# Performance work log

Hardware: AMD Instinct MI355X
Metric: run time of the kernel (lower is better)

## Reference

```python
import jax, jax.numpy as jnp
import numpy as np

BITS = (2, 4, 6, 8, 12, 16)
INIT_S = (0.5, 0.1, 0.05, 0.01, 0.005, 0.001)


def _round_ste(x):
    # straight-through round (LSQ)
    return x + jax.lax.stop_gradient(jnp.round(x) - x)


def _grad_scale(s, g):
    # forward = s, backward grad scaled by g (LSQ grad-scale trick)
    return s * g + jax.lax.stop_gradient(s - s * g)


def _lsq(x, s, num_bits):
    qn = -(2 ** (num_bits - 1))
    qp = 2 ** (num_bits - 1) - 1
    g = 1.0 / float(np.sqrt(x.size * qp))
    ss = _grad_scale(s, g)
    return _round_ste(jnp.clip(x / ss, qn, qp)) * ss


def _gumbel_hard(key, logits, tau):
    u = jax.random.uniform(key, logits.shape, minval=1e-10, maxval=1.0)
    gn = -jnp.log(-jnp.log(u))
    y_soft = jax.nn.softmax((logits + gn) / tau, axis=-1)
    y_hard = jax.nn.one_hot(jnp.argmax(y_soft, axis=-1), logits.shape[-1], dtype=y_soft.dtype)
    return y_hard + y_soft - jax.lax.stop_gradient(y_soft)


def setup_inputs() -> dict:
    key = jax.random.key(0)
    ks = jax.random.split(key, 16)
    B, L, N, K, HD = 64, 256, 8, 64, 64
    inp = {
        "v": jax.random.normal(ks[0], (B, L, K, 2), jnp.float32),
        "H": jax.random.normal(ks[1], (B, L, N, K, 2), jnp.float32),
        "y": jax.random.normal(ks[2], (B, L, N, 2), jnp.float32),
        "local_snr": jax.random.uniform(ks[3], (B, L, K, 1), jnp.float32),
        "w1": jax.random.normal(ks[4], (HD, 9), jnp.float32) * 0.05,
        "b1": jnp.zeros((HD,), jnp.float32),
        "w2": jax.random.normal(ks[5], (HD, HD), jnp.float32) * 0.05,
        "b2": jnp.zeros((HD,), jnp.float32),
        "w3": jax.random.normal(ks[6], (HD, HD), jnp.float32) * 0.05,
        "b3": jnp.zeros((HD,), jnp.float32),
        "wy": jax.random.normal(ks[7], (6, HD), jnp.float32) * 0.05,
        "by": jnp.zeros((6,), jnp.float32),
        "wh": jax.random.normal(ks[8], (6, HD), jnp.float32) * 0.05,
        "bh": jnp.zeros((6,), jnp.float32),
        "wd": jax.random.normal(ks[9], (6, HD), jnp.float32) * 0.05,
        "bd": jnp.zeros((6,), jnp.float32),
        "s_y": jnp.asarray(INIT_S, jnp.float32),
        "s_H": jnp.asarray(INIT_S, jnp.float32),
        "s_d": jnp.asarray(INIT_S, jnp.float32),
        "tau": 1,
    }
    return inp


def reference(v, H, y, local_snr, w1, b1, w2, b2, w3, b3, wy, by, wh, bh, wd, bd, s_y, s_H, s_d, tau):
    tau = float(tau)
    B, L, K, _ = v.shape
    N = H.shape[2]

    v_real = v[..., 0:1]
    v_imag = v[..., 1:2]
    h_power = (H ** 2).sum(axis=(2, 4))                       # (B,L,K)
    channel_norm = h_power[..., None]
    avg_channel_power = jnp.broadcast_to(h_power.mean(axis=1, keepdims=True), (B, L, K))[..., None]
    total_power = h_power.sum(axis=2, keepdims=True)          # (B,L,1)
    interference = total_power - h_power
    sir = jnp.log1p(h_power / (interference + 1e-10))[..., None]
    total_power_norm = jnp.broadcast_to(jnp.log1p(total_power), (B, L, K))[..., None]
    y_power_per_ap = (y ** 2).sum(axis=(2, 3))                # (B,L)
    y_power = jnp.broadcast_to(jnp.log1p(y_power_per_ap)[:, :, None, None], (B, L, K, 1))
    signal_power = jnp.sqrt(v_real ** 2 + v_imag ** 2 + 1e-10)

    feat = jnp.concatenate([v_real, v_imag, local_snr, channel_norm, avg_channel_power,
                            sir, total_power_norm, y_power, signal_power], axis=-1)  # (B,L,K,9)

    h = jax.nn.relu(feat @ w1.T + b1)
    h = jax.nn.relu(h @ w2.T + b2)
    h = jax.nn.relu(h @ w3.T + b3)
    logits_y = h @ wy.T + by
    logits_H = h @ wh.T + bh
    logits_d = h @ wd.T + bd

    logits_y_per_ap = logits_y.mean(axis=2)                   # (B,L,6)
    gkey = jax.random.key(42)
    g1, g2, g3 = jax.random.split(gkey, 3)
    w_y = _gumbel_hard(g1, logits_y_per_ap, tau)              # (B,L,6)
    w_H = _gumbel_hard(g2, logits_H, tau)                     # (B,L,K,6)
    w_demod = _gumbel_hard(g3, logits_d, tau)                 # (B,L,K,6)

    y_stack = jnp.stack([_lsq(y, s_y[i], BITS[i]) for i in range(6)], axis=2)   # (B,L,6,N,2)
    y_q = (y_stack * w_y[:, :, :, None, None]).sum(axis=2)

    H_stack = jnp.stack([_lsq(H, s_H[i], BITS[i]) for i in range(6)], axis=4)   # (B,L,N,K,6,2)
    H_q = (H_stack * w_H[:, :, None, :, :, None]).sum(axis=4)

    v_stack = jnp.stack([_lsq(v, s_d[i], BITS[i]) for i in range(6)], axis=3)   # (B,L,K,6,2)
    v_q = (v_stack * w_demod[..., None]).sum(axis=3)

    bit_values = jnp.asarray([2.0, 4.0, 6.0, 8.0, 12.0, 16.0], v.dtype)
    y_bits_per_ap = 2.0 * N * (w_y * bit_values).sum(axis=-1)                   # (B,L)
    y_bits_per_link = y_bits_per_ap[..., None] / K
    H_bits_per_link = 2.0 * N * (w_H * bit_values).sum(axis=-1)                 # (B,L,K)
    demod_bits_per_link = 2.0 * (w_demod * bit_values).sum(axis=-1)             # (B,L,K)
    expected_bits = y_bits_per_link + H_bits_per_link + demod_bits_per_link

    return (v_q, H_q, y_q, expected_bits, w_y, w_H, w_demod,
            y_bits_per_ap, H_bits_per_link, demod_bits_per_link)
```

## Files before the change

### kernel.cpp

```cpp
#include <hip/hip_runtime.h>
#include <cstdint>


#define JAX_PARTITIONABLE 1

constexpr int BL = 64 * 256;

constexpr long long O_vq  = 0;
constexpr long long O_Hq  = 2097152;
constexpr long long O_yq  = 18874368;
constexpr long long O_eb  = 19136512;
constexpr long long O_wy  = 20185088;
constexpr long long O_wH  = 20283392;
constexpr long long O_wd  = 26574848;
constexpr long long O_yba = 32866304;
constexpr long long O_Hbl = 32882688;
constexpr long long O_dbl = 33931264;

constexpr long long F_SAMPLE = 0;
constexpr long long F_M      = 1048576;

#define MARGIN_THETA 3e-4

__device__ __forceinline__ uint32_t rotl32(uint32_t v, int d) {
  return (v << d) | (v >> (32 - d));
}

__device__ __forceinline__ void threefry2x32(uint32_t k0, uint32_t k1,
                                             uint32_t x0, uint32_t x1,
                                             uint32_t& o0, uint32_t& o1) {
  const uint32_t ks2 = k0 ^ k1 ^ 0x1BD11BDAu;
  x0 += k0; x1 += k1;
  x0 += x1; x1 = rotl32(x1, 13); x1 ^= x0;
  x0 += x1; x1 = rotl32(x1, 15); x1 ^= x0;
  x0 += x1; x1 = rotl32(x1, 26); x1 ^= x0;
  x0 += x1; x1 = rotl32(x1, 6);  x1 ^= x0;
  x0 += k1; x1 += ks2 + 1u;
  x0 += x1; x1 = rotl32(x1, 17); x1 ^= x0;
  x0 += x1; x1 = rotl32(x1, 29); x1 ^= x0;
  x0 += x1; x1 = rotl32(x1, 16); x1 ^= x0;
  x0 += x1; x1 = rotl32(x1, 24); x1 ^= x0;
  x0 += ks2; x1 += k0 + 2u;
  x0 += x1; x1 = rotl32(x1, 13); x1 ^= x0;
  x0 += x1; x1 = rotl32(x1, 15); x1 ^= x0;
  x0 += x1; x1 = rotl32(x1, 26); x1 ^= x0;
  x0 += x1; x1 = rotl32(x1, 6);  x1 ^= x0;
  x0 += k0; x1 += k1 + 3u;
  x0 += x1; x1 = rotl32(x1, 17); x1 ^= x0;
  x0 += x1; x1 = rotl32(x1, 29); x1 ^= x0;
  x0 += x1; x1 = rotl32(x1, 16); x1 ^= x0;
  x0 += x1; x1 = rotl32(x1, 24); x1 ^= x0;
  x0 += k1; x1 += ks2 + 4u;
  x0 += x1; x1 = rotl32(x1, 13); x1 ^= x0;
  x0 += x1; x1 = rotl32(x1, 15); x1 ^= x0;
  x0 += x1; x1 = rotl32(x1, 26); x1 ^= x0;
  x0 += x1; x1 = rotl32(x1, 6);  x1 ^= x0;
  x0 += ks2; x1 += k0 + 5u;
  o0 = x0; o1 = x1;
}

__device__ __forceinline__ uint32_t jax_randbits(uint32_t k0, uint32_t k1,
                                                 uint32_t e, uint32_t size) {
#if JAX_PARTITIONABLE
  (void)size;
  uint32_t o0, o1;
  threefry2x32(k0, k1, 0u, e, o0, o1);
  return o0 ^ o1;
#else
  const uint32_t half = size >> 1;
  uint32_t o0, o1;
  if (e < half) { threefry2x32(k0, k1, e, e + half, o0, o1); return o0; }
  threefry2x32(k0, k1, e - half, e, o0, o1); return o1;
#endif
}

__device__ __forceinline__ float bits_to_unif(uint32_t bits) {
  float f = __uint_as_float((bits >> 9) | 0x3f800000u) - 1.0f;
  return fmaxf(1e-10f, f + 1e-10f);
}

__device__ __forceinline__ double wave_sum_f64(double x) {
#pragma unroll
  for (int off = 32; off > 0; off >>= 1) x += __shfl_xor(x, off);
  return x;
}

__device__ __forceinline__ void argmax_gap6(const double* s, int& arg, double& gap) {
  int a = 0;
#pragma unroll
  for (int j = 1; j < 6; ++j) if (s[j] > s[a]) a = j;
  double second = -1e300;
#pragma unroll
  for (int j = 0; j < 6; ++j) if (j != a && s[j] > second) second = s[j];
  arg = a; gap = s[a] - second;
}

__device__ __forceinline__ float idx_to_bits(int i) {
  return (float)((i < 4) ? 2 * (i + 1) : (i == 4 ? 12 : 16));
}

__global__ void k0_setup(const float* __restrict__ sy, const float* __restrict__ sH,
                         const float* __restrict__ sd, float* __restrict__ ss,
                         uint32_t* __restrict__ keys) {
  const int t = threadIdx.x;
  if (t < 18) {
    const int tensor = t / 6, i = t % 6;
    const int qp_[6] = {1, 7, 31, 127, 2047, 32767};
    const long long sizes[3] = {262144LL, 16777216LL, 2097152LL};
    const float* sarr = tensor == 0 ? sy : (tensor == 1 ? sH : sd);
    const double g64 = 1.0 / sqrt((double)(sizes[tensor] * (long long)qp_[i]));
    const float g32 = (float)g64;
    const float s = sarr[i];
    const float t1 = s * g32;
    ss[t] = t1 + (s - t1);
  }
#if JAX_PARTITIONABLE
  if (t >= 32 && t < 35) {
    uint32_t o0, o1;
    threefry2x32(0u, 42u, 0u, (uint32_t)(t - 32), o0, o1);
    keys[(t - 32) * 2 + 0] = o0;
    keys[(t - 32) * 2 + 1] = o1;
  }
#else
  if (t == 32) {
    uint32_t a0, b0, a1, b1, a2, b2;
    threefry2x32(0u, 42u, 0u, 3u, a0, b0);
    threefry2x32(0u, 42u, 1u, 4u, a1, b1);
    threefry2x32(0u, 42u, 2u, 5u, a2, b2);
    keys[0] = a0; keys[1] = a1;
    keys[2] = a2; keys[3] = b0;
    keys[4] = b1; keys[5] = b2;
  }
#endif
}

__global__ __launch_bounds__(128) void k1a_hpower_partial(
    const float* __restrict__ Hm, double* __restrict__ partial) {
  const int blk = blockIdx.x;
  const int b = blk >> 3, lc = blk & 7;
  const int t = threadIdx.x;
  const float* base = Hm + (size_t)(b * 256 + lc * 32) * 1024;
  double acc = 0.0;
  for (int l = 0; l < 32; ++l) {
#pragma unroll
    for (int n = 0; n < 8; ++n) {
      const float x = base[(size_t)l * 1024 + n * 128 + t];
      acc = fma((double)x, (double)x, acc);
    }
  }
  const double other = __shfl_xor(acc, 1);
  if ((t & 1) == 0) partial[(size_t)blk * 64 + (t >> 1)] = acc + other;
}

__global__ void k1b_hpmean(const double* __restrict__ partial,
                           double* __restrict__ hp_mean) {
  const int id = blockIdx.x * blockDim.x + threadIdx.x;
  if (id >= 4096) return;
  const int b = id >> 6, k = id & 63;
  double s = 0.0;
#pragma unroll
  for (int lc = 0; lc < 8; ++lc) s += partial[(size_t)(b * 8 + lc) * 64 + k];
  hp_mean[id] = s * (1.0 / 256.0);
}

template <int NI, bool RELU>
__device__ __forceinline__ void gemm64(const float* __restrict__ inT,
                                       const float* __restrict__ WT,
                                       const float* __restrict__ bias,
                                       float* __restrict__ outT, int t) {
  const int k0 = (t & 15) * 4;
  const int j0 = (t >> 4) * 4;
  float acc[16];
#pragma unroll
  for (int jj = 0; jj < 4; ++jj) {
    const float bj = bias[j0 + jj];
#pragma unroll
    for (int kk = 0; kk < 4; ++kk) acc[jj * 4 + kk] = bj;
  }
#pragma unroll 16
  for (int i = 0; i < NI; ++i) {
    const float4 x  = *(const float4*)&inT[i * 68 + k0];
    const float4 wv = *(const float4*)&WT[i * 64 + j0];
    acc[0]  = fmaf(wv.x, x.x, acc[0]);
    acc[1]  = fmaf(wv.x, x.y, acc[1]);
    acc[2]  = fmaf(wv.x, x.z, acc[2]);
    acc[3]  = fmaf(wv.x, x.w, acc[3]);
    acc[4]  = fmaf(wv.y, x.x, acc[4]);
    acc[5]  = fmaf(wv.y, x.y, acc[5]);
    acc[6]  = fmaf(wv.y, x.z, acc[6]);
    acc[7]  = fmaf(wv.y, x.w, acc[7]);
    acc[8]  = fmaf(wv.z, x.x, acc[8]);
    acc[9]  = fmaf(wv.z, x.y, acc[9]);
    acc[10] = fmaf(wv.z, x.z, acc[10]);
    acc[11] = fmaf(wv.z, x.w, acc[11]);
    acc[12] = fmaf(wv.w, x.x, acc[12]);
    acc[13] = fmaf(wv.w, x.y, acc[13]);
    acc[14] = fmaf(wv.w, x.z, acc[14]);
    acc[15] = fmaf(wv.w, x.w, acc[15]);
  }
#pragma unroll
  for (int jj = 0; jj < 4; ++jj) {
    float4 r;
    r.x = acc[jj * 4 + 0];
    r.y = acc[jj * 4 + 1];
    r.z = acc[jj * 4 + 2];
    r.w = acc[jj * 4 + 3];
    if (RELU) {
      r.x = fmaxf(r.x, 0.0f); r.y = fmaxf(r.y, 0.0f);
      r.z = fmaxf(r.z, 0.0f); r.w = fmaxf(r.w, 0.0f);
    }
    *(float4*)&outT[(j0 + jj) * 68 + k0] = r;
  }
}

template <int NI>
__device__ __forceinline__ void gemm64_f64(const double* __restrict__ inT,
                                           const float* __restrict__ WT,
                                           const float* __restrict__ bias,
                                           double* __restrict__ outT, int t) {
  const int k0 = (t & 15) * 4;
  const int j0 = (t >> 4) * 4;
  double acc[16];
#pragma unroll
  for (int jj = 0; jj < 4; ++jj) {
    const double bj = (double)bias[j0 + jj];
#pragma unroll
    for (int kk = 0; kk < 4; ++kk) acc[jj * 4 + kk] = bj;
  }
#pragma unroll 8
  for (int i = 0; i < NI; ++i) {
    const double x0 = inT[i * 68 + k0 + 0];
    const double x1 = inT[i * 68 + k0 + 1];
    const double x2 = inT[i * 68 + k0 + 2];
    const double x3 = inT[i * 68 + k0 + 3];
    const float4 wf = *(const float4*)&WT[i * 64 + j0];
    const double w0 = (double)wf.x, w1 = (double)wf.y;
    const double w2 = (double)wf.z, w3 = (double)wf.w;
    acc[0]  = fma(w0, x0, acc[0]);
    acc[1]  = fma(w0, x1, acc[1]);
    acc[2]  = fma(w0, x2, acc[2]);
    acc[3]  = fma(w0, x3, acc[3]);
    acc[4]  = fma(w1, x0, acc[4]);
    acc[5]  = fma(w1, x1, acc[5]);
    acc[6]  = fma(w1, x2, acc[6]);
    acc[7]  = fma(w1, x3, acc[7]);
    acc[8]  = fma(w2, x0, acc[8]);
    acc[9]  = fma(w2, x1, acc[9]);
    acc[10] = fma(w2, x2, acc[10]);
    acc[11] = fma(w2, x3, acc[11]);
    acc[12] = fma(w3, x0, acc[12]);
    acc[13] = fma(w3, x1, acc[13]);
    acc[14] = fma(w3, x2, acc[14]);
    acc[15] = fma(w3, x3, acc[15]);
  }
#pragma unroll
  for (int jj = 0; jj < 4; ++jj) {
#pragma unroll
    for (int kk = 0; kk < 4; ++kk) {
      const double a = acc[jj * 4 + kk];
      outT[(j0 + jj) * 68 + k0 + kk] = a > 0.0 ? a : 0.0;
    }
  }
}

__device__ __forceinline__ void heads20(const float* __restrict__ actT,
                                        const float* __restrict__ whT,
                                        const float* __restrict__ by,
                                        const float* __restrict__ bh,
                                        const float* __restrict__ bd,
                                        float* __restrict__ headP, int t) {
  const int k = t & 63, w = t >> 6;
  float acc[5];
#pragma unroll
  for (int q = 0; q < 5; ++q) {
    const int r = w + 4 * q;
    acc[q] = (r < 6) ? by[r] : (r < 12) ? bh[r - 6] : (r < 18) ? bd[r - 12] : 0.0f;
  }
#pragma unroll 8
  for (int i = 0; i < 64; ++i) {
    const float x = actT[i * 68 + k];
#pragma unroll
    for (int q = 0; q < 5; ++q)
      acc[q] = fmaf(x, whT[(w + 4 * q) * 64 + i], acc[q]);
  }
#pragma unroll
  for (int q = 0; q < 5; ++q) {
    const int r = w + 4 * q;
    if (r < 18) headP[k * 20 + r] = acc[q];
  }
}

__device__ __forceinline__ void heads20_f64(const double* __restrict__ actT,
                                            const float* __restrict__ whT,
                                            const float* __restrict__ by,
                                            const float* __restrict__ bh,
                                            const float* __restrict__ bd,
                                            double* __restrict__ headP, int t) {
  const int k = t & 63, w = t >> 6;
  double acc[5];
#pragma unroll
  for (int q = 0; q < 5; ++q) {
    const int r = w + 4 * q;
    acc[q] = (r < 6) ? (double)by[r]
           : (r < 12) ? (double)bh[r - 6]
           : (r < 18) ? (double)bd[r - 12] : 0.0;
  }
#pragma unroll 8
  for (int i = 0; i < 64; ++i) {
    const double x = actT[i * 68 + k];
#pragma unroll
    for (int q = 0; q < 5; ++q)
      acc[q] = fma(x, (double)whT[(w + 4 * q) * 64 + i], acc[q]);
  }
#pragma unroll
  for (int q = 0; q < 5; ++q) {
    const int r = w + 4 * q;
    if (r < 18) headP[k * 20 + r] = acc[q];
  }
}

__global__ __launch_bounds__(256, 2) void k2_main(
    const float* __restrict__ v, const float* __restrict__ Hm,
    const float* __restrict__ y, const float* __restrict__ snr,
    const float* __restrict__ w1, const float* __restrict__ b1,
    const float* __restrict__ w2, const float* __restrict__ b2,
    const float* __restrict__ w3, const float* __restrict__ b3,
    const float* __restrict__ wy, const float* __restrict__ by,
    const float* __restrict__ wh, const float* __restrict__ bh,
    const float* __restrict__ wd, const float* __restrict__ bd,
    const double* __restrict__ hp_mean, const uint32_t* __restrict__ keys,
    float* __restrict__ out) {
  const int t = threadIdx.x;
  const int lane = t & 63;
  const int wvx = t >> 6;
  const int m0 = blockIdx.x * 4;

  __shared__ __align__(16) float smem[20032];
  float* w1T   = smem;
  float* w2T   = smem + 576;
  float* w3T   = smem + 4672;
  float* whT   = smem + 8768;
  float* actA  = smem + 10048;
  float* actB  = smem + 14400;
  float* headP = smem + 18752;
  double* hp4  = (double*)actB;

  for (int idx = t; idx < 576; idx += 256) {
    const int i = idx >> 6, j = idx & 63;
    w1T[idx] = w1[j * 9 + i];
  }
  for (int idx = t; idx < 4096; idx += 256) {
    const int i = idx >> 6, j = idx & 63;
    w2T[idx] = w2[j * 64 + i];
    w3T[idx] = w3[j * 64 + i];
  }
  for (int idx = t; idx < 1280; idx += 256) {
    const int r = idx >> 6, i = idx & 63;
    whT[idx] = (r < 6) ? wy[r * 64 + i]
             : (r < 12) ? wh[(r - 6) * 64 + i]
             : (r < 18) ? wd[(r - 12) * 64 + i] : 0.0f;
  }

  float ly[6], lh[6], ld[6];
#pragma unroll 1
  for (int mc = 0; mc < 4; ++mc) {
    const int m = m0 + mc;
    {
      const float2* Hp = (const float2*)Hm + (size_t)m * 512;
      double acc = 0.0;
#pragma unroll
      for (int nn = 0; nn < 2; ++nn) {
        const float2 h2v = Hp[(2 * wvx + nn) * 64 + lane];
        acc = fma((double)h2v.x, (double)h2v.x, acc);
        acc = fma((double)h2v.y, (double)h2v.y, acc);
      }
      __syncthreads();
      hp4[wvx * 64 + lane] = acc;
    }
    __syncthreads();

    if (wvx == mc) {
      const double hp = ((hp4[lane] + hp4[64 + lane]) + hp4[128 + lane]) + hp4[192 + lane];
      const double tp = wave_sum_f64(hp);
      double ypart = 0.0;
      if (lane < 16) { const double yv = (double)y[m * 16 + lane]; ypart = yv * yv; }
      const double yp = wave_sum_f64(ypart);
      const float2 vv = ((const float2*)v)[m * 64 + lane];
      const float snrv = snr[m * 64 + lane];
      const double hpm = hp_mean[(m >> 8) * 64 + lane];
      float f[9];
      f[0] = (float)vv.x;
      f[1] = (float)vv.y;
      f[2] = snrv;
      f[3] = (float)hp;
      f[4] = (float)hpm;
      f[5] = (float)log1p(hp / ((tp - hp) + 1e-10));
      f[6] = (float)log1p(tp);
      f[7] = (float)log1p(yp);
      f[8] = (float)sqrt(fma((double)vv.x, (double)vv.x,
                             fma((double)vv.y, (double)vv.y, 1e-10)));
#pragma unroll
      for (int i = 0; i < 9; ++i) actA[i * 68 + lane] = f[i];
    }
    __syncthreads();

    gemm64<9, true>(actA, w1T, b1, actB, t);
    __syncthreads();
    gemm64<64, true>(actB, w2T, b2, actA, t);
    __syncthreads();
    gemm64<64, true>(actA, w3T, b3, actB, t);
    __syncthreads();
    heads20(actB, whT, by, bh, bd, headP, t);
    __syncthreads();

    if (wvx == mc) {
#pragma unroll
      for (int j = 0; j < 6; ++j) {
        ly[j] = headP[lane * 20 + j];
        lh[j] = headP[lane * 20 + 6 + j];
        ld[j] = headP[lane * 20 + 12 + j];
      }
    }
  }

  const int m = m0 + wvx;
  const int k = lane;

  const uint32_t g1k0 = keys[0], g1k1 = keys[1];
  const uint32_t g2k0 = keys[2], g2k1 = keys[3];
  const uint32_t g3k0 = keys[4], g3k1 = keys[5];

  double sH[6], sD[6];
  const uint32_t eH = (uint32_t)(m * 64 + k) * 6u;
#pragma unroll
  for (int j = 0; j < 6; ++j) {
    const float u = bits_to_unif(jax_randbits(g2k0, g2k1, eH + j, 6291456u));
    sH[j] = (double)lh[j] + (double)(-logf(-logf(u)));
  }
#pragma unroll
  for (int j = 0; j < 6; ++j) {
    const float u = bits_to_unif(jax_randbits(g3k0, g3k1, eH + j, 6291456u));
    sD[j] = (double)ld[j] + (double)(-logf(-logf(u)));
  }
  int argH, argD; double gapH, gapD;
  argmax_gap6(sH, argH, gapH);
  argmax_gap6(sD, argD, gapD);

  double lysum[6];
#pragma unroll
  for (int j = 0; j < 6; ++j) lysum[j] = wave_sum_f64((double)ly[j]);

  int argY = 0; double gapY = 1e30;
  if (k == 0) {
    double sY[6];
#pragma unroll
    for (int j = 0; j < 6; ++j) {
      const float u = bits_to_unif(jax_randbits(g1k0, g1k1, (uint32_t)(m * 6 + j), 98304u));
      sY[j] = lysum[j] * (1.0 / 64.0) - log(-log((double)u));
    }
    argmax_gap6(sY, argY, gapY);
  }
  const int needY = __shfl((k == 0 && gapY < MARGIN_THETA) ? 1 : 0, 0);
  const bool fH = gapH < MARGIN_THETA;
  const bool fD = gapD < MARGIN_THETA;

  uint8_t* flags = (uint8_t*)(out + O_vq);
  flags[F_SAMPLE + (size_t)m * 64 + k] = (uint8_t)((fH ? 1 : 0) | (fD ? 2 : 0));
  const bool anyHD = __ballot(fH || fD) != 0ull;
  if (k == 0)
    flags[F_M + m] = (uint8_t)(((anyHD || needY) ? 1 : 0) | (needY ? 2 : 0));

  argY = __shfl(argY, 0);

  const float bY = 16.0f * idx_to_bits(argY);
  const float bH = 16.0f * idx_to_bits(argH);
  const float bD = 2.0f * idx_to_bits(argD);

  if (k == 0) {
    out[O_yba + m] = bY;
#pragma unroll
    for (int j = 0; j < 6; ++j) out[O_wy + m * 6 + j] = (j == argY) ? 1.0f : 0.0f;
  }
  out[O_Hbl + (size_t)m * 64 + k] = bH;
  out[O_dbl + (size_t)m * 64 + k] = bD;
  out[O_eb + (size_t)m * 64 + k] = (bY * 0.015625f + bH) + bD;
#pragma unroll
  for (int j = 0; j < 6; ++j) {
    out[O_wH + (size_t)(m * 64 + k) * 6 + j] = (j == argH) ? 1.0f : 0.0f;
    out[O_wd + (size_t)(m * 64 + k) * 6 + j] = (j == argD) ? 1.0f : 0.0f;
  }
}

__global__ __launch_bounds__(256, 1) void kfix(
    const float* __restrict__ v, const float* __restrict__ Hm,
    const float* __restrict__ y, const float* __restrict__ snr,
    const float* __restrict__ w1, const float* __restrict__ b1,
    const float* __restrict__ w2, const float* __restrict__ b2,
    const float* __restrict__ w3, const float* __restrict__ b3,
    const float* __restrict__ wy, const float* __restrict__ by,
    const float* __restrict__ wh, const float* __restrict__ bh,
    const float* __restrict__ wd, const float* __restrict__ bd,
    const double* __restrict__ hp_mean, const uint32_t* __restrict__ keys,
    float* __restrict__ out) {
  const int t = threadIdx.x;
  const int lane = t & 63;
  const int wvx = t >> 6;
  const int m0 = blockIdx.x * 8;
  const uint8_t* flags = (const uint8_t*)(out + O_vq);

  __shared__ uint32_t mfs[8];
  __shared__ __align__(32) char smem[120064];
  float*  w1T     = (float*)smem;
  float*  w2T     = (float*)(smem + 2304);
  float*  w3T     = (float*)(smem + 18688);
  float*  whT     = (float*)(smem + 35072);
  double* actA64  = (double*)(smem + 40192);
  double* actB64  = (double*)(smem + 75008);
  double* headP64 = (double*)(smem + 109824);
  double* hp4     = actB64;

  if (t < 8) mfs[t] = flags[F_M + m0 + t];
  __syncthreads();
  bool any = false;
#pragma unroll
  for (int i = 0; i < 8; ++i) any |= (mfs[i] != 0);
  if (!any) return;

  for (int idx = t; idx < 576; idx += 256) {
    const int i = idx >> 6, j = idx & 63;
    w1T[idx] = w1[j * 9 + i];
  }
  for (int idx = t; idx < 4096; idx += 256) {
    const int i = idx >> 6, j = idx & 63;
    w2T[idx] = w2[j * 64 + i];
    w3T[idx] = w3[j * 64 + i];
  }
  for (int idx = t; idx < 1280; idx += 256) {
    const int r = idx >> 6, i = idx & 63;
    whT[idx] = (r < 6) ? wy[r * 64 + i]
             : (r < 12) ? wh[(r - 6) * 64 + i]
             : (r < 18) ? wd[(r - 12) * 64 + i] : 0.0f;
  }

#pragma unroll 1
  for (int mi = 0; mi < 8; ++mi) {
    const uint32_t mf = mfs[mi];
    if (mf == 0) continue;
    const int m = m0 + mi;

    {
      const float2* Hp = (const float2*)Hm + (size_t)m * 512;
      double acc = 0.0;
#pragma unroll
      for (int nn = 0; nn < 2; ++nn) {
        const float2 h2v = Hp[(2 * wvx + nn) * 64 + lane];
        acc = fma((double)h2v.x, (double)h2v.x, acc);
        acc = fma((double)h2v.y, (double)h2v.y, acc);
      }
      __syncthreads();
      hp4[wvx * 64 + lane] = acc;
    }
    __syncthreads();

    if (t < 64) {
      const double hp = ((hp4[lane] + hp4[64 + lane]) + hp4[128 + lane]) + hp4[192 + lane];
      const double tp = wave_sum_f64(hp);
      double ypart = 0.0;
      if (lane < 16) { const double yv = (double)y[m * 16 + lane]; ypart = yv * yv; }
      const double yp = wave_sum_f64(ypart);
      const float2 vv = ((const float2*)v)[m * 64 + lane];
      const float snrv = snr[m * 64 + lane];
      const double hpm = hp_mean[(m >> 8) * 64 + lane];
      double f[9];
      f[0] = (double)vv.x;
      f[1] = (double)vv.y;
      f[2] = (double)snrv;
      f[3] = hp;
      f[4] = hpm;
      f[5] = log1p(hp / ((tp - hp) + 1e-10));
      f[6] = log1p(tp);
      f[7] = log1p(yp);
      f[8] = sqrt(fma((double)vv.x, (double)vv.x,
                      fma((double)vv.y, (double)vv.y, 1e-10)));
#pragma unroll
      for (int i = 0; i < 9; ++i) actA64[i * 68 + lane] = f[i];
    }
    __syncthreads();

    gemm64_f64<9>(actA64, w1T, b1, actB64, t);
    __syncthreads();
    gemm64_f64<64>(actB64, w2T, b2, actA64, t);
    __syncthreads();
    gemm64_f64<64>(actA64, w3T, b3, actB64, t);
    __syncthreads();
    heads20_f64(actB64, whT, by, bh, bd, headP64, t);
    __syncthreads();

    if (t < 64) {
      const int k = lane;
      const uint8_t f = flags[F_SAMPLE + (size_t)m * 64 + k];
      double lyd[6], lhd[6], ldd[6];
#pragma unroll
      for (int j = 0; j < 6; ++j) {
        lyd[j] = headP64[k * 20 + j];
        lhd[j] = headP64[k * 20 + 6 + j];
        ldd[j] = headP64[k * 20 + 12 + j];
      }
      const uint32_t g1k0 = keys[0], g1k1 = keys[1];
      const uint32_t g2k0 = keys[2], g2k1 = keys[3];
      const uint32_t g3k0 = keys[4], g3k1 = keys[5];
      const uint32_t eH = (uint32_t)(m * 64 + k) * 6u;

      float bHf, bDf;
      if (f & 1) {
        double s2[6];
#pragma unroll
        for (int j = 0; j < 6; ++j) {
          const float u = bits_to_unif(jax_randbits(g2k0, g2k1, eH + j, 6291456u));
          s2[j] = lhd[j] - log(-log((double)u));
        }
        int argH; double g; argmax_gap6(s2, argH, g);
        bHf = 16.0f * idx_to_bits(argH);
        out[O_Hbl + (size_t)m * 64 + k] = bHf;
#pragma unroll
        for (int j = 0; j < 6; ++j)
          out[O_wH + (size_t)(m * 64 + k) * 6 + j] = (j == argH) ? 1.0f : 0.0f;
      } else {
        bHf = out[O_Hbl + (size_t)m * 64 + k];
      }
      if (f & 2) {
        double s2[6];
#pragma unroll
        for (int j = 0; j < 6; ++j) {
          const float u = bits_to_unif(jax_randbits(g3k0, g3k1, eH + j, 6291456u));
          s2[j] = ldd[j] - log(-log((double)u));
        }
        int argD; double g; argmax_gap6(s2, argD, g);
        bDf = 2.0f * idx_to_bits(argD);
        out[O_dbl + (size_t)m * 64 + k] = bDf;
#pragma unroll
        for (int j = 0; j < 6; ++j)
          out[O_wd + (size_t)(m * 64 + k) * 6 + j] = (j == argD) ? 1.0f : 0.0f;
      } else {
        bDf = out[O_dbl + (size_t)m * 64 + k];
      }

      float bYf;
      if (mf & 2) {
        double lys2[6];
#pragma unroll
        for (int j = 0; j < 6; ++j) lys2[j] = wave_sum_f64(lyd[j]);
        int argY = 0;
        if (k == 0) {
          double s2[6];
#pragma unroll
          for (int j = 0; j < 6; ++j) {
            const float u = bits_to_unif(jax_randbits(g1k0, g1k1, (uint32_t)(m * 6 + j), 98304u));
            s2[j] = lys2[j] * (1.0 / 64.0) - log(-log((double)u));
          }
          double g; argmax_gap6(s2, argY, g);
        }
        argY = __shfl(argY, 0);
        bYf = 16.0f * idx_to_bits(argY);
        if (k == 0) {
          out[O_yba + m] = bYf;
#pragma unroll
          for (int j = 0; j < 6; ++j) out[O_wy + m * 6 + j] = (j == argY) ? 1.0f : 0.0f;
        }
      } else {
        bYf = out[O_yba + m];
      }

      out[O_eb + (size_t)m * 64 + k] = (bYf * 0.015625f + bHf) + bDf;
    }
    __syncthreads();
  }
}

__device__ __forceinline__ int bits_to_idx(int bits) {
  return (bits <= 8) ? ((bits >> 1) - 1) : ((bits == 12) ? 4 : 5);
}

__device__ __forceinline__ float lsq1(float x, float ssv, float qn, float qp) {
  float t = x / ssv;
  t = fminf(fmaxf(t, qn), qp);
  return rintf(t) * ssv;
}

__global__ void k3_Hq(const float* __restrict__ Hm, const float* __restrict__ ss,
                      const float* __restrict__ Hbits, float* __restrict__ outHq) {
  const int id = blockIdx.x * blockDim.x + threadIdx.x;
  if (id >= 8388608) return;
  const int k = id & 63;
  const int m = id >> 9;
  const int bits = (int)Hbits[(size_t)m * 64 + k] >> 4;
  const int i = bits_to_idx(bits);
  const float ssv = ss[6 + i];
  const float qp = (float)((1 << (bits - 1)) - 1);
  const float qn = -(float)(1 << (bits - 1));
  const float2 x = ((const float2*)Hm)[id];
  float2 o;
  o.x = lsq1(x.x, ssv, qn, qp);
  o.y = lsq1(x.y, ssv, qn, qp);
  ((float2*)outHq)[id] = o;
}

__global__ void k4_vq(const float* __restrict__ v, const float* __restrict__ ss,
                      const float* __restrict__ dbits, float* __restrict__ outvq) {
  const int id = blockIdx.x * blockDim.x + threadIdx.x;
  if (id >= 1048576) return;
  const int bits = (int)dbits[id] >> 1;
  const int i = bits_to_idx(bits);
  const float ssv = ss[12 + i];
  const float qp = (float)((1 << (bits - 1)) - 1);
  const float qn = -(float)(1 << (bits - 1));
  const float2 x = ((const float2*)v)[id];
  float2 o;
  o.x = lsq1(x.x, ssv, qn, qp);
  o.y = lsq1(x.y, ssv, qn, qp);
  ((float2*)outvq)[id] = o;
}

__global__ void k5_yq(const float* __restrict__ y, const float* __restrict__ ss,
                      const float* __restrict__ ybits, float* __restrict__ outyq) {
  const int id = blockIdx.x * blockDim.x + threadIdx.x;
  if (id >= 131072) return;
  const int m = id >> 3;
  const int bits = (int)ybits[m] >> 4;
  const int i = bits_to_idx(bits);
  const float ssv = ss[i];
  const float qp = (float)((1 << (bits - 1)) - 1);
  const float qn = -(float)(1 << (bits - 1));
  const float2 x = ((const float2*)y)[id];
  float2 o;
  o.x = lsq1(x.x, ssv, qn, qp);
  o.y = lsq1(x.y, ssv, qn, qp);
  ((float2*)outyq)[id] = o;
}

extern "C" void kernel_launch(void* const* d_in, const int* in_sizes, int n_in,
                              void* d_out, int out_size, void* d_ws, size_t ws_size,
                              hipStream_t stream) {
  const float* v   = (const float*)d_in[0];
  const float* Hm  = (const float*)d_in[1];
  const float* y   = (const float*)d_in[2];
  const float* snr = (const float*)d_in[3];
  const float* w1  = (const float*)d_in[4];
  const float* b1  = (const float*)d_in[5];
  const float* w2  = (const float*)d_in[6];
  const float* b2  = (const float*)d_in[7];
  const float* w3  = (const float*)d_in[8];
  const float* b3  = (const float*)d_in[9];
  const float* wy  = (const float*)d_in[10];
  const float* by  = (const float*)d_in[11];
  const float* wh  = (const float*)d_in[12];
  const float* bh  = (const float*)d_in[13];
  const float* wd  = (const float*)d_in[14];
  const float* bd  = (const float*)d_in[15];
  const float* sy  = (const float*)d_in[16];
  const float* sH  = (const float*)d_in[17];
  const float* sd  = (const float*)d_in[18];

  float* out = (float*)d_out;

  double* ws_partial = (double*)d_ws;
  double* ws_hpmean  = ws_partial + 32768;
  float*  ws_ss      = (float*)(ws_hpmean + 4096);
  uint32_t* ws_keys  = (uint32_t*)(ws_ss + 18);

  k0_setup<<<1, 64, 0, stream>>>(sy, sH, sd, ws_ss, ws_keys);
  k1a_hpower_partial<<<512, 128, 0, stream>>>(Hm, ws_partial);
  k1b_hpmean<<<16, 256, 0, stream>>>(ws_partial, ws_hpmean);
  k2_main<<<BL / 4, 256, 0, stream>>>(v, Hm, y, snr, w1, b1, w2, b2, w3, b3,
                                      wy, by, wh, bh, wd, bd, ws_hpmean, ws_keys, out);
  kfix<<<BL / 8, 256, 0, stream>>>(v, Hm, y, snr, w1, b1, w2, b2, w3, b3,
                                   wy, by, wh, bh, wd, bd, ws_hpmean, ws_keys, out);
  k3_Hq<<<32768, 256, 0, stream>>>(Hm, ws_ss, out + O_Hbl, out + O_Hq);
  k4_vq<<<4096, 256, 0, stream>>>(v, ws_ss, out + O_dbl, out + O_vq);
  k5_yq<<<512, 256, 0, stream>>>(y, ws_ss, out + O_yba, out + O_yq);
}
```

Before: 857.6 us.

## Give each wave its own sample in the MLP kernel with pre-transposed weights

The MLP kernel used to loop over four samples per block, with all four waves computing each sample together and a block-wide barrier between layers. Now each wave runs its own sample's MLP on a private XOR-swizzled LDS buffer, with an 8x8 register tile per lane and only wave-local waits between layers. The weight transposes move into a separate small kernel that writes them into the H_q output area, which a later kernel overwrites. The per-block transpose and most of the barriers go away, at the cost of 64 accumulators per thread and weights read from global/L2 instead of LDS.

```diff
diff --git a/kernel.cpp b/kernel.cpp
--- a/kernel.cpp
+++ b/kernel.cpp
@@ -99,6 +99,8 @@
   return (float)((i < 4) ? 2 * (i + 1) : (i == 4 ? 12 : 16));
 }
 
+#define WSYNC() asm volatile("s_waitcnt lgkmcnt(0)" ::: "memory")
+
 __global__ void k0_setup(const float* __restrict__ sy, const float* __restrict__ sH,
                          const float* __restrict__ sd, float* __restrict__ ss,
                          uint32_t* __restrict__ keys) {
@@ -134,6 +136,25 @@
 #endif
 }
 
+__global__ void k0w_transpose(const float* __restrict__ w1, const float* __restrict__ w2,
+                              const float* __restrict__ w3, const float* __restrict__ wy,
+                              const float* __restrict__ wh, const float* __restrict__ wd,
+                              float* __restrict__ wsT) {
+  const int t = blockIdx.x * blockDim.x + threadIdx.x;
+  for (int idx = t; idx < 576; idx += 4096)
+    wsT[idx] = w1[(idx & 63) * 9 + (idx >> 6)];
+  for (int idx = t; idx < 4096; idx += 4096) {
+    wsT[576 + idx]  = w2[(idx & 63) * 64 + (idx >> 6)];
+    wsT[4672 + idx] = w3[(idx & 63) * 64 + (idx >> 6)];
+  }
+  for (int idx = t; idx < 2048; idx += 4096) {
+    const int i = idx >> 5, r = idx & 31;
+    wsT[8768 + idx] = (r < 6) ? wy[r * 64 + i]
+                    : (r < 12) ? wh[(r - 6) * 64 + i]
+                    : (r < 18) ? wd[(r - 12) * 64 + i] : 0.0f;
+  }
+}
+
 __global__ __launch_bounds__(128) void k1a_hpower_partial(
     const float* __restrict__ Hm, double* __restrict__ partial) {
   const int blk = blockIdx.x;
@@ -164,52 +185,230 @@
 }
 
 template <int NI, bool RELU>
-__device__ __forceinline__ void gemm64(const float* __restrict__ inT,
-                                       const float* __restrict__ WT,
-                                       const float* __restrict__ bias,
-                                       float* __restrict__ outT, int t) {
-  const int k0 = (t & 15) * 4;
-  const int j0 = (t >> 4) * 4;
-  float acc[16];
-#pragma unroll
-  for (int jj = 0; jj < 4; ++jj) {
-    const float bj = bias[j0 + jj];
-#pragma unroll
-    for (int kk = 0; kk < 4; ++kk) acc[jj * 4 + kk] = bj;
-  }
-#pragma unroll 16
+__device__ __forceinline__ void wgemm(float* act, const float* __restrict__ Wg,
+                                      const float* __restrict__ bias, int lane) {
+  const int a = lane >> 3, b = lane & 7;
+  const int j0 = a * 8, k0 = b * 8;
+  float acc[64];
+  {
+    const float4 bj0 = *(const float4*)(bias + j0);
+    const float4 bj1 = *(const float4*)(bias + j0 + 4);
+    const float bjv[8] = {bj0.x, bj0.y, bj0.z, bj0.w, bj1.x, bj1.y, bj1.z, bj1.w};
+#pragma unroll
+    for (int jj = 0; jj < 8; ++jj)
+#pragma unroll
+      for (int kk = 0; kk < 8; ++kk) acc[jj * 8 + kk] = bjv[jj];
+  }
+#pragma unroll 4
   for (int i = 0; i < NI; ++i) {
-    const float4 x  = *(const float4*)&inT[i * 68 + k0];
-    const float4 wv = *(const float4*)&WT[i * 64 + j0];
-    acc[0]  = fmaf(wv.x, x.x, acc[0]);
-    acc[1]  = fmaf(wv.x, x.y, acc[1]);
-    acc[2]  = fmaf(wv.x, x.z, acc[2]);
-    acc[3]  = fmaf(wv.x, x.w, acc[3]);
-    acc[4]  = fmaf(wv.y, x.x, acc[4]);
-    acc[5]  = fmaf(wv.y, x.y, acc[5]);
-    acc[6]  = fmaf(wv.y, x.z, acc[6]);
-    acc[7]  = fmaf(wv.y, x.w, acc[7]);
-    acc[8]  = fmaf(wv.z, x.x, acc[8]);
-    acc[9]  = fmaf(wv.z, x.y, acc[9]);
-    acc[10] = fmaf(wv.z, x.z, acc[10]);
-    acc[11] = fmaf(wv.z, x.w, acc[11]);
-    acc[12] = fmaf(wv.w, x.x, acc[12]);
-    acc[13] = fmaf(wv.w, x.y, acc[13]);
-    acc[14] = fmaf(wv.w, x.z, acc[14]);
-    acc[15] = fmaf(wv.w, x.w, acc[15]);
-  }
-#pragma unroll
-  for (int jj = 0; jj < 4; ++jj) {
-    float4 r;
-    r.x = acc[jj * 4 + 0];
-    r.y = acc[jj * 4 + 1];
-    r.z = acc[jj * 4 + 2];
-    r.w = acc[jj * 4 + 3];
+    const int sw = (i * 64 + k0) ^ (((i >> 3) & 7) << 2);
+    const float4 xa = *(const float4*)(act + sw);
+    const float4 xb = *(const float4*)(act + (sw ^ 4));
+    const float4 wa = *(const float4*)(Wg + i * 64 + j0);
+    const float4 wb = *(const float4*)(Wg + i * 64 + j0 + 4);
+    const float xv[8] = {xa.x, xa.y, xa.z, xa.w, xb.x, xb.y, xb.z, xb.w};
+    const float wv[8] = {wa.x, wa.y, wa.z, wa.w, wb.x, wb.y, wb.z, wb.w};
+#pragma unroll
+    for (int jj = 0; jj < 8; ++jj)
+#pragma unroll
+      for (int kk = 0; kk < 8; ++kk)
+        acc[jj * 8 + kk] = fmaf(wv[jj], xv[kk], acc[jj * 8 + kk]);
+  }
+  asm volatile("" ::: "memory");
+#pragma unroll
+  for (int jj = 0; jj < 8; ++jj) {
+    const int j = j0 + jj;
+    const int swo = (j * 64 + k0) ^ ((a & 7) << 2);
+    float4 r0, r1;
+    r0.x = acc[jj * 8 + 0]; r0.y = acc[jj * 8 + 1];
+    r0.z = acc[jj * 8 + 2]; r0.w = acc[jj * 8 + 3];
+    r1.x = acc[jj * 8 + 4]; r1.y = acc[jj * 8 + 5];
+    r1.z = acc[jj * 8 + 6]; r1.w = acc[jj * 8 + 7];
     if (RELU) {
-      r.x = fmaxf(r.x, 0.0f); r.y = fmaxf(r.y, 0.0f);
-      r.z = fmaxf(r.z, 0.0f); r.w = fmaxf(r.w, 0.0f);
-    }
-    *(float4*)&outT[(j0 + jj) * 68 + k0] = r;
+      r0.x = fmaxf(r0.x, 0.0f); r0.y = fmaxf(r0.y, 0.0f);
+      r0.z = fmaxf(r0.z, 0.0f); r0.w = fmaxf(r0.w, 0.0f);
+      r1.x = fmaxf(r1.x, 0.0f); r1.y = fmaxf(r1.y, 0.0f);
+      r1.z = fmaxf(r1.z, 0.0f); r1.w = fmaxf(r1.w, 0.0f);
+    }
+    *(float4*)(act + swo) = r0;
+    *(float4*)(act + (swo ^ 4)) = r1;
+  }
+}
+
+__device__ __forceinline__ void wheads(float* buf, const float* __restrict__ whT,
+                                       const float* __restrict__ hb, int lane) {
+  const int r0 = (lane >> 4) * 5;
+  const int k0 = (lane & 15) * 4;
+  float acc[20];
+#pragma unroll
+  for (int q = 0; q < 5; ++q) {
+    const float bq = hb[r0 + q];
+#pragma unroll
+    for (int kk = 0; kk < 4; ++kk) acc[q * 4 + kk] = bq;
+  }
+#pragma unroll 4
+  for (int i = 0; i < 64; ++i) {
+    const int sw = (i * 64 + k0) ^ (((i >> 3) & 7) << 2);
+    const float4 x = *(const float4*)(buf + sw);
+#pragma unroll
+    for (int q = 0; q < 5; ++q) {
+      const float w = whT[i * 32 + r0 + q];
+      acc[q * 4 + 0] = fmaf(x.x, w, acc[q * 4 + 0]);
+      acc[q * 4 + 1] = fmaf(x.y, w, acc[q * 4 + 1]);
+      acc[q * 4 + 2] = fmaf(x.z, w, acc[q * 4 + 2]);
+      acc[q * 4 + 3] = fmaf(x.w, w, acc[q * 4 + 3]);
+    }
+  }
+  asm volatile("" ::: "memory");
+#pragma unroll
+  for (int q = 0; q < 5; ++q)
+#pragma unroll
+    for (int kk = 0; kk < 4; ++kk)
+      buf[(k0 + kk) * 20 + r0 + q] = acc[q * 4 + kk];
+}
+
+__global__ __launch_bounds__(256, 2) void k2_main(
+    const float* __restrict__ v, const float* __restrict__ Hm,
+    const float* __restrict__ y, const float* __restrict__ snr,
+    const float* __restrict__ b1, const float* __restrict__ b2,
+    const float* __restrict__ b3, const float* __restrict__ by,
+    const float* __restrict__ bh, const float* __restrict__ bd,
+    const float* __restrict__ wsT, const double* __restrict__ hp_mean,
+    const uint32_t* __restrict__ keys, float* __restrict__ out) {
+  const int t = threadIdx.x;
+  const int lane = t & 63;
+  const int wvx = t >> 6;
+  const int m = blockIdx.x * 4 + wvx;
+
+  __shared__ __align__(16) float smem[18464];
+  float* whT = smem + 16384;
+  float* hb  = smem + 18432;
+  float* buf = smem + wvx * 4096;
+
+  for (int idx = t; idx < 2048; idx += 256) whT[idx] = wsT[8768 + idx];
+  if (t < 20)
+    hb[t] = (t < 6) ? by[t] : (t < 12) ? bh[t - 6] : (t < 18) ? bd[t - 12] : 0.0f;
+  __syncthreads();
+
+  {
+    const float2* Hp = (const float2*)Hm + (size_t)m * 512;
+    double aw[4];
+#pragma unroll
+    for (int w = 0; w < 4; ++w) {
+      double acc = 0.0;
+#pragma unroll
+      for (int nn = 0; nn < 2; ++nn) {
+        const float2 h2v = Hp[(2 * w + nn) * 64 + lane];
+        acc = fma((double)h2v.x, (double)h2v.x, acc);
+        acc = fma((double)h2v.y, (double)h2v.y, acc);
+      }
+      aw[w] = acc;
+    }
+    const double hp = ((aw[0] + aw[1]) + aw[2]) + aw[3];
+    const double tp = wave_sum_f64(hp);
+    double ypart = 0.0;
+    if (lane < 16) { const double yv = (double)y[m * 16 + lane]; ypart = yv * yv; }
+    const double yp = wave_sum_f64(ypart);
+    const float2 vv = ((const float2*)v)[m * 64 + lane];
+    const float snrv = snr[m * 64 + lane];
+    const double hpm = hp_mean[(m >> 8) * 64 + lane];
+    float f[9];
+    f[0] = (float)vv.x;
+    f[1] = (float)vv.y;
+    f[2] = snrv;
+    f[3] = (float)hp;
+    f[4] = (float)hpm;
+    f[5] = (float)log1p(hp / ((tp - hp) + 1e-10));
+    f[6] = (float)log1p(tp);
+    f[7] = (float)log1p(yp);
+    f[8] = (float)sqrt(fma((double)vv.x, (double)vv.x,
+                           fma((double)vv.y, (double)vv.y, 1e-10)));
+#pragma unroll
+    for (int i = 0; i < 9; ++i)
+      buf[(i * 64 + lane) ^ (((i >> 3) & 7) << 2)] = f[i];
+  }
+  WSYNC();
+  wgemm<9, true>(buf, wsT, b1, lane);
+  WSYNC();
+  wgemm<64, true>(buf, wsT + 576, b2, lane);
+  WSYNC();
+  wgemm<64, true>(buf, wsT + 4672, b3, lane);
+  WSYNC();
+  wheads(buf, whT, hb, lane);
+  WSYNC();
+
+  float ly[6], lh[6], ld[6];
+#pragma unroll
+  for (int j = 0; j < 6; ++j) {
+    ly[j] = buf[lane * 20 + j];
+    lh[j] = buf[lane * 20 + 6 + j];
+    ld[j] = buf[lane * 20 + 12 + j];
+  }
+
+  const int k = lane;
+
+  const uint32_t g1k0 = keys[0], g1k1 = keys[1];
+  const uint32_t g2k0 = keys[2], g2k1 = keys[3];
+  const uint32_t g3k0 = keys[4], g3k1 = keys[5];
+
+  double sH[6], sD[6];
+  const uint32_t eH = (uint32_t)(m * 64 + k) * 6u;
+#pragma unroll
+  for (int j = 0; j < 6; ++j) {
+    const float u = bits_to_unif(jax_randbits(g2k0, g2k1, eH + j, 6291456u));
+    sH[j] = (double)lh[j] + (double)(-logf(-logf(u)));
+  }
+#pragma unroll
+  for (int j = 0; j < 6; ++j) {
+    const float u = bits_to_unif(jax_randbits(g3k0, g3k1, eH + j, 6291456u));
+    sD[j] = (double)ld[j] + (double)(-logf(-logf(u)));
+  }
+  int argH, argD; double gapH, gapD;
+  argmax_gap6(sH, argH, gapH);
+  argmax_gap6(sD, argD, gapD);
+
+  double lysum[6];
+#pragma unroll
+  for (int j = 0; j < 6; ++j) lysum[j] = wave_sum_f64((double)ly[j]);
+
+  int argY = 0; double gapY = 1e30;
+  if (k == 0) {
+    double sY[6];
+#pragma unroll
+    for (int j = 0; j < 6; ++j) {
+      const float u = bits_to_unif(jax_randbits(g1k0, g1k1, (uint32_t)(m * 6 + j), 98304u));
+      sY[j] = lysum[j] * (1.0 / 64.0) - log(-log((double)u));
+    }
+    argmax_gap6(sY, argY, gapY);
+  }
+  const int needY = __shfl((k == 0 && gapY < MARGIN_THETA) ? 1 : 0, 0);
+  const bool fH = gapH < MARGIN_THETA;
+  const bool fD = gapD < MARGIN_THETA;
+
+  uint8_t* flags = (uint8_t*)(out + O_vq);
+  flags[F_SAMPLE + (size_t)m * 64 + k] = (uint8_t)((fH ? 1 : 0) | (fD ? 2 : 0));
+  const bool anyHD = __ballot(fH || fD) != 0ull;
+  if (k == 0)
+    flags[F_M + m] = (uint8_t)(((anyHD || needY) ? 1 : 0) | (needY ? 2 : 0));
+
+  argY = __shfl(argY, 0);
+
+  const float bY = 16.0f * idx_to_bits(argY);
+  const float bH = 16.0f * idx_to_bits(argH);
+  const float bD = 2.0f * idx_to_bits(argD);
+
+  if (k == 0) {
+    out[O_yba + m] = bY;
+#pragma unroll
+    for (int j = 0; j < 6; ++j) out[O_wy + m * 6 + j] = (j == argY) ? 1.0f : 0.0f;
+  }
+  out[O_Hbl + (size_t)m * 64 + k] = bH;
+  out[O_dbl + (size_t)m * 64 + k] = bD;
+  out[O_eb + (size_t)m * 64 + k] = (bY * 0.015625f + bH) + bD;
+#pragma unroll
+  for (int j = 0; j < 6; ++j) {
+    out[O_wH + (size_t)(m * 64 + k) * 6 + j] = (j == argH) ? 1.0f : 0.0f;
+    out[O_wd + (size_t)(m * 64 + k) * 6 + j] = (j == argD) ? 1.0f : 0.0f;
   }
 }
 
@@ -263,33 +462,6 @@
   }
 }
 
-__device__ __forceinline__ void heads20(const float* __restrict__ actT,
-                                        const float* __restrict__ whT,
-                                        const float* __restrict__ by,
-                                        const float* __restrict__ bh,
-                                        const float* __restrict__ bd,
-                                        float* __restrict__ headP, int t) {
-  const int k = t & 63, w = t >> 6;
-  float acc[5];
-#pragma unroll
-  for (int q = 0; q < 5; ++q) {
-    const int r = w + 4 * q;
-    acc[q] = (r < 6) ? by[r] : (r < 12) ? bh[r - 6] : (r < 18) ? bd[r - 12] : 0.0f;
-  }
-#pragma unroll 8
-  for (int i = 0; i < 64; ++i) {
-    const float x = actT[i * 68 + k];
-#pragma unroll
-    for (int q = 0; q < 5; ++q)
-      acc[q] = fmaf(x, whT[(w + 4 * q) * 64 + i], acc[q]);
-  }
-#pragma unroll
-  for (int q = 0; q < 5; ++q) {
-    const int r = w + 4 * q;
-    if (r < 18) headP[k * 20 + r] = acc[q];
-  }
-}
-
 __device__ __forceinline__ void heads20_f64(const double* __restrict__ actT,
                                             const float* __restrict__ whT,
                                             const float* __restrict__ by,
@@ -316,178 +488,6 @@
   for (int q = 0; q < 5; ++q) {
     const int r = w + 4 * q;
     if (r < 18) headP[k * 20 + r] = acc[q];
-  }
-}
-
-__global__ __launch_bounds__(256, 2) void k2_main(
-    const float* __restrict__ v, const float* __restrict__ Hm,
-    const float* __restrict__ y, const float* __restrict__ snr,
-    const float* __restrict__ w1, const float* __restrict__ b1,
-    const float* __restrict__ w2, const float* __restrict__ b2,
-    const float* __restrict__ w3, const float* __restrict__ b3,
-    const float* __restrict__ wy, const float* __restrict__ by,
-    const float* __restrict__ wh, const float* __restrict__ bh,
-    const float* __restrict__ wd, const float* __restrict__ bd,
-    const double* __restrict__ hp_mean, const uint32_t* __restrict__ keys,
-    float* __restrict__ out) {
-  const int t = threadIdx.x;
-  const int lane = t & 63;
-  const int wvx = t >> 6;
-  const int m0 = blockIdx.x * 4;
-
-  __shared__ __align__(16) float smem[20032];
-  float* w1T   = smem;
-  float* w2T   = smem + 576;
-  float* w3T   = smem + 4672;
-  float* whT   = smem + 8768;
-  float* actA  = smem + 10048;
-  float* actB  = smem + 14400;
-  float* headP = smem + 18752;
-  double* hp4  = (double*)actB;
-
-  for (int idx = t; idx < 576; idx += 256) {
-    const int i = idx >> 6, j = idx & 63;
-    w1T[idx] = w1[j * 9 + i];
-  }
-  for (int idx = t; idx < 4096; idx += 256) {
-    const int i = idx >> 6, j = idx & 63;
-    w2T[idx] = w2[j * 64 + i];
-    w3T[idx] = w3[j * 64 + i];
-  }
-  for (int idx = t; idx < 1280; idx += 256) {
-    const int r = idx >> 6, i = idx & 63;
-    whT[idx] = (r < 6) ? wy[r * 64 + i]
-             : (r < 12) ? wh[(r - 6) * 64 + i]
-             : (r < 18) ? wd[(r - 12) * 64 + i] : 0.0f;
-  }
-
-  float ly[6], lh[6], ld[6];
-#pragma unroll 1
-  for (int mc = 0; mc < 4; ++mc) {
-    const int m = m0 + mc;
-    {
-      const float2* Hp = (const float2*)Hm + (size_t)m * 512;
-      double acc = 0.0;
-#pragma unroll
-      for (int nn = 0; nn < 2; ++nn) {
-        const float2 h2v = Hp[(2 * wvx + nn) * 64 + lane];
-        acc = fma((double)h2v.x, (double)h2v.x, acc);
-        acc = fma((double)h2v.y, (double)h2v.y, acc);
-      }
-      __syncthreads();
-      hp4[wvx * 64 + lane] = acc;
-    }
-    __syncthreads();
-
-    if (wvx == mc) {
-      const double hp = ((hp4[lane] + hp4[64 + lane]) + hp4[128 + lane]) + hp4[192 + lane];
-      const double tp = wave_sum_f64(hp);
-      double ypart = 0.0;
-      if (lane < 16) { const double yv = (double)y[m * 16 + lane]; ypart = yv * yv; }
-      const double yp = wave_sum_f64(ypart);
-      const float2 vv = ((const float2*)v)[m * 64 + lane];
-      const float snrv = snr[m * 64 + lane];
-      const double hpm = hp_mean[(m >> 8) * 64 + lane];
-      float f[9];
-      f[0] = (float)vv.x;
-      f[1] = (float)vv.y;
-      f[2] = snrv;
-      f[3] = (float)hp;
-      f[4] = (float)hpm;
-      f[5] = (float)log1p(hp / ((tp - hp) + 1e-10));
-      f[6] = (float)log1p(tp);
-      f[7] = (float)log1p(yp);
-      f[8] = (float)sqrt(fma((double)vv.x, (double)vv.x,
-                             fma((double)vv.y, (double)vv.y, 1e-10)));
-#pragma unroll
-      for (int i = 0; i < 9; ++i) actA[i * 68 + lane] = f[i];
-    }
-    __syncthreads();
-
-    gemm64<9, true>(actA, w1T, b1, actB, t);
-    __syncthreads();
-    gemm64<64, true>(actB, w2T, b2, actA, t);
-    __syncthreads();
-    gemm64<64, true>(actA, w3T, b3, actB, t);
-    __syncthreads();
-    heads20(actB, whT, by, bh, bd, headP, t);
-    __syncthreads();
-
-    if (wvx == mc) {
-#pragma unroll
-      for (int j = 0; j < 6; ++j) {
-        ly[j] = headP[lane * 20 + j];
-        lh[j] = headP[lane * 20 + 6 + j];
-        ld[j] = headP[lane * 20 + 12 + j];
-      }
-    }
-  }
-
-  const int m = m0 + wvx;
-  const int k = lane;
-
-  const uint32_t g1k0 = keys[0], g1k1 = keys[1];
-  const uint32_t g2k0 = keys[2], g2k1 = keys[3];
-  const uint32_t g3k0 = keys[4], g3k1 = keys[5];
-
-  double sH[6], sD[6];
-  const uint32_t eH = (uint32_t)(m * 64 + k) * 6u;
-#pragma unroll
-  for (int j = 0; j < 6; ++j) {
-    const float u = bits_to_unif(jax_randbits(g2k0, g2k1, eH + j, 6291456u));
-    sH[j] = (double)lh[j] + (double)(-logf(-logf(u)));
-  }
-#pragma unroll
-  for (int j = 0; j < 6; ++j) {
-    const float u = bits_to_unif(jax_randbits(g3k0, g3k1, eH + j, 6291456u));
-    sD[j] = (double)ld[j] + (double)(-logf(-logf(u)));
-  }
-  int argH, argD; double gapH, gapD;
-  argmax_gap6(sH, argH, gapH);
-  argmax_gap6(sD, argD, gapD);
-
-  double lysum[6];
-#pragma unroll
-  for (int j = 0; j < 6; ++j) lysum[j] = wave_sum_f64((double)ly[j]);
-
-  int argY = 0; double gapY = 1e30;
-  if (k == 0) {
-    double sY[6];
-#pragma unroll
-    for (int j = 0; j < 6; ++j) {
-      const float u = bits_to_unif(jax_randbits(g1k0, g1k1, (uint32_t)(m * 6 + j), 98304u));
-      sY[j] = lysum[j] * (1.0 / 64.0) - log(-log((double)u));
-    }
-    argmax_gap6(sY, argY, gapY);
-  }
-  const int needY = __shfl((k == 0 && gapY < MARGIN_THETA) ? 1 : 0, 0);
-  const bool fH = gapH < MARGIN_THETA;
-  const bool fD = gapD < MARGIN_THETA;
-
-  uint8_t* flags = (uint8_t*)(out + O_vq);
-  flags[F_SAMPLE + (size_t)m * 64 + k] = (uint8_t)((fH ? 1 : 0) | (fD ? 2 : 0));
-  const bool anyHD = __ballot(fH || fD) != 0ull;
-  if (k == 0)
-    flags[F_M + m] = (uint8_t)(((anyHD || needY) ? 1 : 0) | (needY ? 2 : 0));
-
-  argY = __shfl(argY, 0);
-
-  const float bY = 16.0f * idx_to_bits(argY);
-  const float bH = 16.0f * idx_to_bits(argH);
-  const float bD = 2.0f * idx_to_bits(argD);
-
-  if (k == 0) {
-    out[O_yba + m] = bY;
-#pragma unroll
-    for (int j = 0; j < 6; ++j) out[O_wy + m * 6 + j] = (j == argY) ? 1.0f : 0.0f;
-  }
-  out[O_Hbl + (size_t)m * 64 + k] = bH;
-  out[O_dbl + (size_t)m * 64 + k] = bD;
-  out[O_eb + (size_t)m * 64 + k] = (bY * 0.015625f + bH) + bD;
-#pragma unroll
-  for (int j = 0; j < 6; ++j) {
-    out[O_wH + (size_t)(m * 64 + k) * 6 + j] = (j == argH) ? 1.0f : 0.0f;
-    out[O_wd + (size_t)(m * 64 + k) * 6 + j] = (j == argD) ? 1.0f : 0.0f;
   }
 }
 
@@ -768,11 +768,14 @@
   float*  ws_ss      = (float*)(ws_hpmean + 4096);
   uint32_t* ws_keys  = (uint32_t*)(ws_ss + 18);
 
+  float* wsT = out + O_Hq;
+
   k0_setup<<<1, 64, 0, stream>>>(sy, sH, sd, ws_ss, ws_keys);
+  k0w_transpose<<<16, 256, 0, stream>>>(w1, w2, w3, wy, wh, wd, wsT);
   k1a_hpower_partial<<<512, 128, 0, stream>>>(Hm, ws_partial);
   k1b_hpmean<<<16, 256, 0, stream>>>(ws_partial, ws_hpmean);
-  k2_main<<<BL / 4, 256, 0, stream>>>(v, Hm, y, snr, w1, b1, w2, b2, w3, b3,
-                                      wy, by, wh, bh, wd, bd, ws_hpmean, ws_keys, out);
+  k2_main<<<BL / 4, 256, 0, stream>>>(v, Hm, y, snr, b1, b2, b3, by, bh, bd,
+                                      wsT, ws_hpmean, ws_keys, out);
   kfix<<<BL / 8, 256, 0, stream>>>(v, Hm, y, snr, w1, b1, w2, b2, w3, b3,
                                    wy, by, wh, bh, wd, bd, ws_hpmean, ws_keys, out);
   k3_Hq<<<32768, 256, 0, stream>>>(Hm, ws_ss, out + O_Hbl, out + O_Hq);
```

After: 725.2 us. 15.4% less time.
